# Optimization experiments

Hardware: AMD Instinct MI355X
Metric: run time of the kernel (lower is better)

## Reference

```python
import jax, jax.numpy as jnp
import numpy as np

L = 4
B_LIST = [30, 17, 9, 5, 3]      # bandwidth schedule (geometric 30 -> 3)
F_LIST = [1, 2, 5, 12, 28, 64]  # channel schedule (geometric 1 -> 64)
BATCH = 32
C64 = jnp.complex64

# near-identity grids (beta = pi/16, 6 alphas; SO3 grid additionally 6 gammas)
_A6 = np.linspace(0.0, 2 * np.pi, 6, endpoint=False)
S2_BETA = np.full(6, np.pi / 16)
S2_ALPHA = _A6
_aa, _gg = np.meshgrid(_A6, _A6, indexing='ij')
SO3_ALPHA = _aa.ravel()
SO3_BETA = np.full(36, np.pi / 16)
SO3_GAMMA = _gg.ravel()


def betas_of(b):
    return np.pi * (2 * np.arange(2 * b) + 1) / (4 * b)


def quad_weights(b):
    j = np.arange(2 * b)
    k = np.arange(b)
    s = (np.sin(np.pi * np.outer(2 * j + 1, 2 * k + 1) / (4 * b)) / (2 * k + 1)).sum(1)
    return (2.0 / b) * np.sin(np.pi * (2 * j + 1) / (4 * b)) * s


def wigner_d_all(lmax, betas):
    """Wigner small-d d^l_{m',m}(beta) via exp(-i beta Jy); list_l of [nbeta,2l+1,2l+1]."""
    out = [np.ones((len(betas), 1, 1))]
    for l in range(1, lmax):
        m = np.arange(-l, l)
        jp = np.sqrt(l * (l + 1) - m * (m + 1))  # <m+1|J+|m>
        Jy = np.zeros((2 * l + 1, 2 * l + 1), np.complex128)
        i = np.arange(2 * l)
        Jy[i + 1, i] = -0.5j * jp
        Jy[i, i + 1] = 0.5j * jp
        lam, U = np.linalg.eigh(Jy)
        ph = np.exp(-1j * np.outer(betas, lam))
        out.append(np.einsum('ak,bk,ck->bac', U, ph, U.conj()).real)
    return out


def fft_idx(l, n):
    # indices of frequencies m = -l..l in fft ordering of length n
    return np.concatenate([np.arange(n - l, n), np.arange(l + 1)])


def s2_fft(x, b_out):
    # x: [B,f,2b,2b] real (beta,alpha) -> list_l of [B,f,2l+1] complex
    b_in = x.shape[-1] // 2
    wig = wigner_d_all(b_out, betas_of(b_in))
    w = quad_weights(b_in)
    xf = jnp.fft.fft(x, axis=-1)
    out = []
    for l in range(b_out):
        dl = jnp.asarray((wig[l][:, :, l] * w[:, None]).astype(np.complex64))  # [2b,2l+1]
        out.append(jnp.einsum('bfjm,jm->bfm', xf[..., fft_idx(l, 2 * b_in)], dl))
    return out


def so3_fft(x, b_out):
    # x: [B,f,2b,2b,2b] real (beta,alpha,gamma) -> list_l of [B,f,2l+1,2l+1]
    b_in = x.shape[-1] // 2
    wig = wigner_d_all(b_out, betas_of(b_in))
    w = quad_weights(b_in)
    xf = jnp.fft.fft2(x, axes=(-2, -1))
    out = []
    for l in range(b_out):
        idx = fft_idx(l, 2 * b_in)
        dl = jnp.asarray((wig[l] * w[:, None, None]).astype(np.complex64))
        out.append(jnp.einsum('bfjmn,jmn->bfmn', xf[:, :, :, idx[:, None], idx[None, :]], dl))
    return out


def so3_ifft(coeffs, b):
    # coeffs: list_l [B,f,2l+1,2l+1] -> real signal [B,f,2b,2b,2b]
    wig = wigner_d_all(b, betas_of(b))
    nb = 2 * b
    Bz, f = coeffs[0].shape[:2]
    X = jnp.zeros((Bz, f, nb, nb, nb), C64)
    for l in range(b):
        idx = fft_idx(l, nb)
        dl = jnp.asarray(((2 * l + 1) * wig[l]).astype(np.complex64))
        X = X.at[:, :, :, idx[:, None], idx[None, :]].add(
            jnp.einsum('bfmn,jmn->bfjmn', coeffs[l], dl))
    return (jnp.fft.ifft2(X, axes=(-2, -1)) * (nb * nb)).real


def s2_kernel_ft(k, b):
    # k: [f_in,f_out,P] -> list_l of [2l+1,f_in,f_out] complex
    wig = wigner_d_all(b, S2_BETA)
    kc = k.astype(C64)
    out = []
    for l in range(b):
        m = np.arange(-l, l + 1)
        F = (wig[l][:, :, l] * np.exp(1j * np.outer(S2_ALPHA, m))).astype(np.complex64)
        out.append(jnp.einsum('iop,pm->mio', kc, jnp.asarray(F)))
    return out


def so3_kernel_ft(k, b):
    # k: [f_in,f_out,P] -> list_l of [2l+1,2l+1,f_in,f_out] complex
    wig = wigner_d_all(b, SO3_BETA)
    kc = k.astype(C64)
    out = []
    for l in range(b):
        m = np.arange(-l, l + 1)
        F = (wig[l]
             * np.exp(1j * np.outer(SO3_ALPHA, m))[:, :, None]
             * np.exp(1j * np.outer(SO3_GAMMA, m))[:, None, :]).astype(np.complex64)
        out.append(jnp.einsum('iop,pmn->mnio', kc, jnp.asarray(F)))
    return out


def s2_conv(x, kern, b_out):
    xh = s2_fft(x, b_out)
    kh = s2_kernel_ft(kern, b_out)
    yh = [jnp.einsum('bim,nio->bomn', xh[l], kh[l].conj()) for l in range(b_out)]
    return so3_ifft(yh, b_out)


def so3_conv(x, kern, b_out):
    xh = so3_fft(x, b_out)
    kh = so3_kernel_ft(kern, b_out)
    yh = [jnp.einsum('bimk,nkio->bomn', xh[l], kh[l].conj()) for l in range(b_out)]
    return so3_ifft(yh, b_out)


def so3_integrate(x):
    b = x.shape[-1] // 2
    w = jnp.asarray(quad_weights(b).astype(np.float32))
    return jnp.einsum('bfjac,j->bf', x, w) / float((2 * b) ** 2)


def batchnorm(x, g, be):
    mu = x.mean(0)
    var = ((x - mu) ** 2).mean(0)
    return (x - mu) * jax.lax.rsqrt(var + 1e-5) * g + be


def setup_inputs() -> dict:
    key = jax.random.key(0)
    ks = jax.random.split(key, 10)
    rn = lambda k, s, sc=1.0: jax.random.normal(k, s, jnp.float32) * sc
    return {
        'x': rn(ks[0], (BATCH, 1, 60, 60)),
        'k_s2': rn(ks[1], (1, 2, 6), 0.5),
        'k1': rn(ks[2], (2, 5, 36), 0.1),
        'k2': rn(ks[3], (5, 12, 36), 0.1),
        'k3': rn(ks[4], (12, 28, 36), 0.1),
        'k4': rn(ks[5], (28, 64, 36), 0.1),
        'g1': jnp.ones(64), 'be1': jnp.zeros(64),
        'w1': rn(ks[6], (64, 64), 0.125), 'b1': jnp.zeros(64),
        'g2': jnp.ones(64), 'be2': jnp.zeros(64),
        'w2': rn(ks[7], (64, 32), 0.125), 'b2': jnp.zeros(32),
        'g3': jnp.ones(32), 'be3': jnp.zeros(32),
        'w3': rn(ks[8], (32, 10), 0.18), 'b3': jnp.zeros(10),
    }


def reference(x, k_s2, k1, k2, k3, k4, g1, be1, w1, b1, g2, be2, w2, b2, g3, be3, w3, b3):
    h = jax.nn.relu(s2_conv(x, k_s2, B_LIST[0]))            # [B,2,60,60,60]
    for k, bo in zip((k1, k2, k3, k4), B_LIST[1:]):
        h = jax.nn.relu(so3_conv(h, k, bo))                 # bandwidth shrinks 17,9,5,3
    h = so3_integrate(h)                                    # [B,64]
    h = jax.nn.relu(batchnorm(h, g1, be1) @ w1 + b1)
    h = jax.nn.relu(batchnorm(h, g2, be2) @ w2 + b2)
    return batchnorm(h, g3, be3) @ w3 + b3                  # [B,10]
```

## Files before the change

kernel.cpp:

```cpp
#include <hip/hip_runtime.h>
#include <cmath>
#include <cstring>
#include <vector>


#define DPI 3.14159265358979323846

static constexpr int OQh(int l) { return l*(4*l*l - 1)/3; }
static_assert(OQh(30) == 35990, "oq30");
static_assert(OQh(17) == 6545,  "oq17");
static_assert(OQh(9)  == 969,   "oq9");
static_assert(OQh(5)  == 165,   "oq5");
static_assert(OQh(3)  == 35,    "oq3");

static constexpr int T1SUM = 18445;
static constexpr int T2SUM = 3417;

static constexpr size_t al256(size_t x){ return (x + 255) & ~(size_t)255; }
static constexpr size_t WS_XF1  = 0;
static constexpr size_t WS_XH1  = WS_XF1  + al256(32ull*60*30*8);
static constexpr size_t WS_KH1  = WS_XH1  + al256(32ull*900*8);
static constexpr size_t WS_XT2  = WS_KH1  + al256(1800ull*8);
static constexpr size_t WS_XH2  = WS_XT2  + al256(561ull*3840*8);
static constexpr size_t WS_KH2  = WS_XH2  + al256(64ull*6545*8);
static constexpr size_t WS_YH2T = WS_KH2  + al256(6545ull*10*8);
static constexpr size_t WS_XT3  = WS_YH2T + al256(6545ull*160*8);
static constexpr size_t WS_XH3  = WS_XT3  + al256(153ull*5440*8);
static constexpr size_t WS_KH3  = WS_XH3  + al256(160ull*969*8);
static constexpr size_t WS_YH3T = WS_KH3  + al256(969ull*60*8);
static constexpr size_t WS_XT4  = WS_YH3T + al256(969ull*384*8);
static constexpr size_t WS_XH4  = WS_XT4  + al256(384ull*18*45*8);
static constexpr size_t WS_KH4  = WS_XH4  + al256(384ull*165*8);
static constexpr size_t WS_YH4T = WS_KH4  + al256(165ull*336*8);
static constexpr size_t WS_XT5  = WS_YH4T + al256(165ull*896*8);
static constexpr size_t WS_XH5  = WS_XT5  + al256(896ull*10*15*8);
static constexpr size_t WS_KH5  = WS_XH5  + al256(896ull*35*8);
static constexpr size_t WS_YH5T = WS_KH5  + al256(35ull*1792*8);
static constexpr size_t WS_S5P  = WS_YH5T + al256(35ull*2048*8);
static constexpr size_t WS_RTM  = WS_S5P  + al256(2048ull*6*4);
static constexpr size_t WS_RU   = WS_RTM  + al256(60ull*30*1920*8);
static constexpr size_t WS_TOTAL= WS_RU   + al256(60ull*17*1920*8);

struct ConstOffs {
  size_t A1, dAT2, dAT3, A4, A5;
  size_t dT1, dT2;
  size_t S3, S4, S5;
  size_t WInt;
  size_t nF;
  size_t Fs2, Fso3;
  size_t Tw60, Tw34, Tw18, Tw10, Tw6;
  size_t Wn1, Wn2o, Wn4, Wn5;
  size_t Wg1, Wg2, Wg4;
  size_t WC1, WC2;
  size_t nC;
};
static ConstOffs CO;
static float*  g_devF = nullptr;
static float2* g_devC = nullptr;
static int*    g_devI = nullptr;
static constexpr int IO_TOFF1 = 0;
static constexpr int IO_TOFF2 = 1770;
static constexpr int IO_QOFF2 = 2331;
static constexpr int IO_QLST2 = 2893;
static constexpr int IO_QOFF3 = 9438;
static constexpr int IO_QLST3 = 9592;
static constexpr int IO_TOTAL = 10561;

static void tqli(double* d, double* e, int n, double* z) {
  e[n-1] = 0.0;
  for (int l = 0; l < n; l++) {
    int iter = 0;
    int m;
    do {
      for (m = l; m < n-1; m++) {
        double dd = fabs(d[m]) + fabs(d[m+1]);
        if (fabs(e[m]) <= 1e-300 + 1e-14*dd) break;
      }
      if (m != l) {
        if (iter++ == 80) break;
        double g = (d[l+1]-d[l])/(2.0*e[l]);
        double r = hypot(g, 1.0);
        g = d[m]-d[l]+e[l]/(g + (g >= 0.0 ? fabs(r) : -fabs(r)));
        double s = 1.0, c = 1.0, p = 0.0;
        int i;
        r = 1.0;
        for (i = m-1; i >= l; i--) {
          double f = s*e[i], b = c*e[i];
          r = hypot(f, g);
          e[i+1] = r;
          if (r == 0.0) { d[i+1] -= p; e[m] = 0.0; break; }
          s = f/r; c = g/r;
          g = d[i+1]-p;
          r = (d[i]-g)*s + 2.0*c*b;
          p = s*r;
          d[i+1] = g+p;
          g = c*r-b;
          for (int k = 0; k < n; k++) {
            f = z[(size_t)k*n+i+1];
            z[(size_t)k*n+i+1] = s*z[(size_t)k*n+i] + c*f;
            z[(size_t)k*n+i]   = c*z[(size_t)k*n+i] - s*f;
          }
        }
        if (r == 0.0 && i >= l) continue;
        d[l] -= p; e[l] = g; e[m] = 0.0;
      }
    } while (m != l);
  }
}

struct Builder {
  std::vector<std::vector<double>> V, Lam;
  bool useExpm[30];

  Builder() {
    V.resize(30); Lam.resize(30);
    for (int l = 0; l < 30; l++) {
      int n = 2*l+1;
      std::vector<double> d(n, 0.0), e(n, 0.0), z((size_t)n*n, 0.0);
      for (int i = 0; i < n; i++) z[(size_t)i*n+i] = 1.0;
      for (int i = 0; i+1 < n; i++) {
        double m = (double)i - l;
        e[i] = -0.5*sqrt((double)l*(l+1) - m*(m+1.0));
      }
      if (n > 1) tqli(d.data(), e.data(), n, z.data());
      V[l] = std::move(z); Lam[l] = std::move(d);
    }
    std::vector<double> t((size_t)59*59);
    for (int l = 0; l < 30; l++) {
      useExpm[l] = false;
      if (l == 0) continue;
      int n = 2*l+1;
      eigD(l, 0.77, t.data());
      double corner = pow(cos(0.385), 2.0*l);
      double err = fabs(t[0] - corner) + fabs(t[(size_t)(n-1)*n + (n-1)] - corner);
      double s = 0.0;
      for (int c = 0; c < n; c++) s += t[c]*t[c];
// ... 16 lines not shown
        const double* f = (r & 1) ? sk : ck;
        double s = 0.0;
        for (int k = 0; k < n; k++) s += va[k]*vc[k]*f[k];
        out[(size_t)a*n + c] = (r >= 2) ? -s : s;
      }
    }
  }

  void expmD(int l, double beta, double* out) {
    int n = 2*l+1;
    int s = 0; double bl = fabs(beta)*(double)l + 1e-12;
    while (bl > 0.25) { bl *= 0.5; s++; }
    double sc = ldexp(beta, -s);
    std::vector<double> sup(n > 1 ? n-1 : 0);
    for (int i = 0; i+1 < n; i++) {
      double m = (double)i - l;
      sup[i] = 0.5*sqrt((double)l*(l+1) - m*(m+1.0))*sc;
    }
    std::vector<double> term((size_t)n*n, 0.0), acc((size_t)n*n, 0.0), t2((size_t)n*n);
    for (int i = 0; i < n; i++) { term[(size_t)i*n+i] = 1.0; acc[(size_t)i*n+i] = 1.0; }
    for (int k = 1; k <= 16; k++) {
      for (int r = 0; r < n; r++)
        for (int c = 0; c < n; c++) {
          double v = 0.0;
          if (c > 0)   v += term[(size_t)r*n + c-1]*sup[c-1];
          if (c+1 < n) v -= term[(size_t)r*n + c+1]*sup[c];
          t2[(size_t)r*n+c] = v/(double)k;
        }
      term.swap(t2);
      for (size_t i2 = 0; i2 < (size_t)n*n; i2++) acc[i2] += term[i2];
    }
    for (int t = 0; t < s; t++) {
      for (int r = 0; r < n; r++)
        for (int c = 0; c < n; c++) {
          double v = 0.0;
          for (int k = 0; k < n; k++) v += acc[(size_t)r*n+k]*acc[(size_t)k*n+c];
          t2[(size_t)r*n+c] = v;
        }
      acc.swap(t2);
    }
    std::memcpy(out, acc.data(), sizeof(double)*(size_t)n*n);
  }

  void buildD(int l, double beta, double* out) {
    if (useExpm[l]) expmD(l, beta, out); else eigD(l, beta, out);
  }
};

static std::vector<double> quadw_h(int b) {
  std::vector<double> w(2*b);
  for (int j = 0; j < 2*b; j++) {
    double s = 0;
    for (int k = 0; k < b; k++)
      s += sin(DPI*(2*j+1)*(2*k+1)/(4.0*b))/(double)(2*k+1);
    w[j] = (2.0/b)*sin(DPI*(2*j+1)/(4.0*b))*s;
  }
  return w;
}

static void build_all() {
  size_t o = 0;
  CO.A1   = o; o += 60ull*900;
  CO.dAT2 = o; o += (size_t)OQh(17)*60;
  CO.dAT3 = o; o += (size_t)OQh(9)*34;
  CO.A4   = o; o += 18ull*OQh(5);
  CO.A5   = o; o += 10ull*OQh(3);
  CO.dT1  = o; o += (size_t)T1SUM*60;
  CO.dT2  = o; o += (size_t)T2SUM*34;
  CO.S3   = o; o += 18ull*OQh(9);
  CO.S4   = o; o += 10ull*OQh(5);
  CO.S5   = o; o +=  6ull*OQh(3);
  CO.WInt = o; o += 8;
  CO.nF = o;
  size_t c = 0;
  CO.Fs2  = c; c += 6ull*900;
  CO.Fso3 = c; c += 36ull*OQh(17);
  CO.Tw60 = c; c += 60; CO.Tw34 = c; c += 34;
  CO.Tw18 = c; c += 18; CO.Tw10 = c; c += 10; CO.Tw6 = c; c += 6;
  CO.Wn1  = c; c += 30*60; CO.Wn2o = c; c += 17*34;
  CO.Wn4  = c; c += 5*10;  CO.Wn5  = c; c += 3*6;
  CO.Wg1  = c; c += 60*17; CO.Wg2  = c; c += 34*9; CO.Wg4 = c; c += 10*3;
  CO.WC1  = c; c += 33*60;
  CO.WC2  = c; c += 17*34;
  CO.nC = c;

  std::vector<float> HF(CO.nF, 0.f);
  std::vector<float> HC(2*CO.nC, 0.f);
  std::vector<int> HI(IO_TOTAL, 0);

  { int acc = 0;
    for (int pm = 0; pm < 59; pm++) for (int n = 0; n < 30; n++) {
      int m = pm - 29, am = m < 0 ? -m : m;
      int lm = am > n ? am : n;
      HI[IO_TOFF1 + pm*30 + n] = acc; acc += 30 - lm;
    } }
  { int acc = 0;
    for (int pm = 0; pm < 33; pm++) for (int n = 0; n < 17; n++) {
      int m = pm - 16, am = m < 0 ? -m : m;
      int lm = am > n ? am : n;
      HI[IO_TOFF2 + pm*17 + n] = acc; acc += 17 - lm;
    } }
  { int pos = 0;
    for (int mh = -16; mh <= 16; mh++)
      for (int kh = 0; kh < 17; kh++) {
        HI[IO_QOFF2 + (mh+16)*17 + kh] = pos;
        int am = mh < 0 ? -mh : mh;
        int lmin = am > kh ? am : kh;
        for (int l = lmin; l < 17; l++) {
          int q = OQh(l) + (mh+l)*(2*l+1) + (kh+l);
          HI[IO_QLST2 + pos++] = q*2;
        }
        if (kh > 0)
          for (int l = lmin; l < 17; l++) {
            int q = OQh(l) + (-mh+l)*(2*l+1) + (-kh+l);
            HI[IO_QLST2 + pos++] = q*2 + 1;
          }
      }
    HI[IO_QOFF2 + 561] = pos;
  }
  { int pos = 0;
    for (int mh = -8; mh <= 8; mh++)
      for (int kh = 0; kh < 9; kh++) {
        HI[IO_QOFF3 + (mh+8)*9 + kh] = pos;
        int am = mh < 0 ? -mh : mh;
        int lmin = am > kh ? am : kh;
        for (int l = lmin; l < 9; l++) {
          int q = OQh(l) + (mh+l)*(2*l+1) + (kh+l);
          HI[IO_QLST3 + pos++] = q*2;
        }
        if (kh > 0)
          for (int l = lmin; l < 9; l++) {
            int q = OQh(l) + (-mh+l)*(2*l+1) + (-kh+l);
            HI[IO_QLST3 + pos++] = q*2 + 1;
          }
      }
    HI[IO_QOFF3 + 153] = pos;
  }

  Builder B;
  auto betas = [](int b){ std::vector<double> v(2*b);
    for (int j = 0; j < 2*b; j++) v[j] = DPI*(2*j+1)/(4.0*b); return v; };
  auto w30 = quadw_h(30), w17 = quadw_h(17), w9 = quadw_h(9), w5 = quadw_h(5), w3 = quadw_h(3);
  std::vector<double> tmp((size_t)59*59);

  { auto bs = betas(30);
    for (int l = 0; l < 30; l++) { int W = 2*l+1;
      for (int j = 0; j < 60; j++) {
        B.buildD(l, bs[j], tmp.data());
        for (int mm = -l; mm <= l; mm++)
          for (int nn = 0; nn <= l; nn++) {
            int am = mm < 0 ? -mm : mm;
            int lmin = am > nn ? am : nn;
            int term = HI[IO_TOFF1 + (mm+29)*30 + nn] + (l - lmin);
            HF[CO.dT1 + (size_t)term*60 + j] =
              (float)((2*l+1)*tmp[(size_t)(mm+l)*W + (nn+l)]);
          }
        if (l < 17) {
          for (int rem = 0; rem < W*W; rem++)
            HF[CO.dAT2 + (size_t)(OQh(l)+rem)*60 + j] = (float)(tmp[rem]*w30[j]);
        }
        float* dA1 = HF.data() + CO.A1 + 60ull*l*l + (size_t)j*W;
        for (int mi = 0; mi < W; mi++) dA1[mi] = (float)(tmp[(size_t)mi*W + l]*w30[j]);
      } } }
  { auto bs = betas(17);
    for (int l = 0; l < 17; l++) { int W = 2*l+1;
      for (int j = 0; j < 34; j++) {
// ... 15 lines not shown
      for (int j = 0; j < 18; j++) {
        B.buildD(l, bs[j], tmp.data());
        float* dst = HF.data() + CO.S3 + 18ull*OQh(l) + (size_t)j*W*W;
        for (int i2 = 0; i2 < W*W; i2++) dst[i2] = (float)((2*l+1)*tmp[i2]);
        if (l < 5) {
          float* dA = HF.data() + CO.A4 + 18ull*OQh(l) + (size_t)j*W*W;
          for (int i2 = 0; i2 < W*W; i2++) dA[i2] = (float)(tmp[i2]*w9[j]);
        } } } }
  { auto bs = betas(5);
    for (int l = 0; l < 5; l++) { int W = 2*l+1;
      for (int j = 0; j < 10; j++) {
        B.buildD(l, bs[j], tmp.data());
        float* dst = HF.data() + CO.S4 + 10ull*OQh(l) + (size_t)j*W*W;
        for (int i2 = 0; i2 < W*W; i2++) dst[i2] = (float)((2*l+1)*tmp[i2]);
        if (l < 3) {
          float* dA = HF.data() + CO.A5 + 10ull*OQh(l) + (size_t)j*W*W;
          for (int i2 = 0; i2 < W*W; i2++) dA[i2] = (float)(tmp[i2]*w5[j]);
        } } } }
  { auto bs = betas(3);
    for (int l = 0; l < 3; l++) { int W = 2*l+1;
      for (int j = 0; j < 6; j++) {
        B.buildD(l, bs[j], tmp.data());
        float* dst = HF.data() + CO.S5 + 6ull*OQh(l) + (size_t)j*W*W;
        for (int i2 = 0; i2 < W*W; i2++) dst[i2] = (float)((2*l+1)*tmp[i2]);
      } } }
  { double beta = DPI/16.0;
    for (int l = 0; l < 30; l++) { int n = 2*l+1;
      B.buildD(l, beta, tmp.data());
      for (int p = 0; p < 6; p++) {
        double al = 2.0*DPI*p/6.0;
        for (int mi = 0; mi < n; mi++) {
          double ph = al*(double)(mi - l);
          double dr = tmp[(size_t)mi*n + l];
          size_t off = CO.Fs2 + 6ull*l*l + (size_t)p*n + mi;
          HC[2*off]   = (float)(dr*cos(ph));
          HC[2*off+1] = (float)(dr*sin(ph));
        } }
      if (l < 17) {
        for (int p = 0; p < 36; p++) {
          double al = 2.0*DPI*(p/6)/6.0, ga = 2.0*DPI*(p%6)/6.0;
          for (int mi = 0; mi < n; mi++)
            for (int ni = 0; ni < n; ni++) {
              double ph = al*(double)(mi - l) + ga*(double)(ni - l);
              double dr = tmp[(size_t)mi*n + ni];
              size_t off = CO.Fso3 + 36ull*OQh(l) + (size_t)p*n*n + (size_t)mi*n + ni;
              HC[2*off]   = (float)(dr*cos(ph));
              HC[2*off+1] = (float)(dr*sin(ph));
            } } } } }
  auto fillTw = [&](size_t ofs, int N){
    for (int t = 0; t < N; t++) {
      HC[2*(ofs+t)]   = (float)cos(2.0*DPI*t/N);
      HC[2*(ofs+t)+1] = (float)sin(2.0*DPI*t/N);
    } };
  fillTw(CO.Tw60, 60); fillTw(CO.Tw34, 34);
  fillTw(CO.Tw18, 18); fillTw(CO.Tw10, 10); fillTw(CO.Tw6, 6);
  auto fillWn = [&](size_t ofs, int BQ, int N){
    for (int n = 0; n < BQ; n++)
      for (int cc2 = 0; cc2 < N; cc2++) {
        double f = (n == 0) ? 1.0 : 2.0;
        HC[2*(ofs + (size_t)n*N + cc2)]   = (float)(f*cos(2.0*DPI*n*cc2/N));
        HC[2*(ofs + (size_t)n*N + cc2)+1] = (float)(f*sin(2.0*DPI*n*cc2/N));
      } };
  auto fillWg = [&](size_t ofs, int N, int KT){
    for (int cc2 = 0; cc2 < N; cc2++)
      for (int k = 0; k < KT; k++) {
        HC[2*(ofs + (size_t)cc2*KT + k)]   = (float)cos(2.0*DPI*k*cc2/N);
        HC[2*(ofs + (size_t)cc2*KT + k)+1] = (float)(-sin(2.0*DPI*k*cc2/N));
      } };
  fillWn(CO.Wn1, 30, 60); fillWn(CO.Wn2o, 17, 34);
  fillWn(CO.Wn4, 5, 10);  fillWn(CO.Wn5, 3, 6);
  fillWg(CO.Wg1, 60, 17); fillWg(CO.Wg2, 34, 9); fillWg(CO.Wg4, 10, 3);
  for (int p = 0; p < 33; p++)
    for (int a = 0; a < 60; a++) {
      double th = 2.0*DPI*(p-16)*a/60.0;
      HC[2*(CO.WC1 + (size_t)p*60 + a)]   = (float)cos(th);
      HC[2*(CO.WC1 + (size_t)p*60 + a)+1] = (float)sin(th);
    }
  for (int p = 0; p < 17; p++)
    for (int a = 0; a < 34; a++) {
      double th = 2.0*DPI*(p-8)*a/34.0;
      HC[2*(CO.WC2 + (size_t)p*34 + a)]   = (float)cos(th);
      HC[2*(CO.WC2 + (size_t)p*34 + a)+1] = (float)sin(th);
    }
  for (int j = 0; j < 6; j++) HF[CO.WInt + j] = (float)(w3[j]/36.0);

  size_t fb  = CO.nF * sizeof(float);
  size_t fbA = al256(fb);
  size_t cb  = CO.nC * sizeof(float2);
  size_t cbA = al256(cb);
  size_t ib  = HI.size() * sizeof(int);
  void* base = nullptr;
  if (hipMalloc(&base, fbA + cbA + ib) != hipSuccess || !base) return;
  if (hipMemcpy(base, HF.data(), fb, hipMemcpyHostToDevice) != hipSuccess) return;
  if (hipMemcpy((char*)base + fbA, HC.data(), cb, hipMemcpyHostToDevice) != hipSuccess) return;
  if (hipMemcpy((char*)base + fbA + cbA, HI.data(), ib, hipMemcpyHostToDevice) != hipSuccess) return;
  (void)hipDeviceSynchronize();
  g_devF = (float*)base;
  g_devC = (float2*)((char*)base + fbA);
  g_devI = (int*)((char*)base + fbA + cbA);
}
namespace { struct InitOnce { InitOnce(){ build_all(); } } g_once; }

__device__ __forceinline__ int OQ(int l) { return l*(4*l*l - 1)/3; }
__device__ __forceinline__ int lFromQ(int q, int L) {
  int l = 0;
  while (l+1 < L && OQ(l+1) <= q) l++;
  return l;
}
__device__ __forceinline__ int lsq(int q) {
  int l = (int)sqrtf((float)q);
  while ((l+1)*(l+1) <= q) l++;
  while (l*l > q) l--;
  return l;
}
__device__ __forceinline__ void rotf(float2& r, float2 s) {
  float t = r.x*s.x - r.y*s.y;
  r.y = r.x*s.y + r.y*s.x;
  r.x = t;
}

__device__ __forceinline__ void kh_so3_one(int id, int L, int fi, int fo,
    const float* __restrict__ kk, const float2* __restrict__ F, float2* __restrict__ kh)
{
  int ff = fi*fo;
  int q = id / ff, r = id - q*ff;
  int i = r / fo, o = r - i*fo;
  int l = lFromQ(q, L); int W = 2*l+1; int W21 = W*W;
  int rem = q - OQ(l);
  const float2* Fb = F + 36ull*OQ(l) + rem;
  const float* kb = kk + (size_t)(i*fo + o)*36;
  float ax = 0.f, ay = 0.f;
  for (int p = 0; p < 36; p++) {
    float kv = kb[p];
    float2 f = Fb[(size_t)p*W21];
    ax += kv*f.x; ay += kv*f.y;
  }
  kh[(size_t)q*ff + r] = make_float2(ax, ay);
}

__global__ __launch_bounds__(256) void k_kh_all(
    const float* __restrict__ ks2, const float* __restrict__ k1,
    const float* __restrict__ k2,  const float* __restrict__ k3,
    const float* __restrict__ k4,
    const float2* __restrict__ Fs2, const float2* __restrict__ Fso3,
    float2* __restrict__ kh1, float2* __restrict__ kh2, float2* __restrict__ kh3,
    float2* __restrict__ kh4, float2* __restrict__ kh5)
{
  int id = blockIdx.x*256 + threadIdx.x;
  if (id < 1800) {
    int q = id >> 1, o = id & 1;
    int l = lsq(q); int W = 2*l+1; int mi = q - l*l;
    const float2* Fb = Fs2 + 6ull*l*l;
    float ax = 0.f, ay = 0.f;
    for (int p = 0; p < 6; p++) {
      float kv = ks2[o*6 + p];
      float2 f = Fb[p*W + mi];
      ax += kv*f.x; ay += kv*f.y;
    }
    kh1[(size_t)q*2 + o] = make_float2(ax, ay);
    return;
  }
  id -= 1800;
  if (id < OQh(17)*10) { kh_so3_one(id, 17, 2, 5, k1, Fso3, kh2); return; }
  id -= OQh(17)*10;
  if (id < OQh(9)*60) { kh_so3_one(id, 9, 5, 12, k2, Fso3, kh3); return; }
  id -= OQh(9)*60;
  if (id < OQh(5)*336) { kh_so3_one(id, 5, 12, 28, k3, Fso3, kh4); return; }
  id -= OQh(5)*336;
  if (id < OQh(3)*1792) { kh_so3_one(id, 3, 28, 64, k4, Fso3, kh5); return; }
}

__global__ __launch_bounds__(64) void k_s1_fftA(
    const float* __restrict__ x, const float2* __restrict__ tw, float2* __restrict__ XF1)
{
  __shared__ float row[60];
  int b = blockIdx.x / 60, j = blockIdx.x - b*60;
  int t = threadIdx.x;
  if (t < 60) row[t] = x[((size_t)b*60 + j)*60 + t];
  __syncthreads();
  if (t < 30) {
    float ax = 0.f, ay = 0.f;
    int ti = 0;
    for (int a = 0; a < 60; a++) {
      float2 w = tw[ti];
      ax += row[a]*w.x; ay -= row[a]*w.y;
      ti += t; if (ti >= 60) ti -= 60;
    }
    XF1[((size_t)b*60 + j)*30 + t] = make_float2(ax, ay);
  }
}

__global__ __launch_bounds__(256) void k_s1_coef(
    const float2* __restrict__ XF1, const float* __restrict__ dA1, float2* __restrict__ xh1)
{
  int id = blockIdx.x*blockDim.x + threadIdx.x;
  if (id >= 32*900) return;
  int b = id / 900, q = id - b*900;
  int l = lsq(q); int W = 2*l+1; int mi = q - l*l; int m = mi - l;
  const float* dp = dA1 + 60ull*l*l + mi;
  const float2* xb = XF1 + (size_t)b*60*30;
  int ma = m >= 0 ? m : -m;
  float sg = m >= 0 ? 1.f : -1.f;
  float ax = 0.f, ay = 0.f;
  for (int j = 0; j < 60; j++) {
    float2 xf = xb[j*30 + ma];
    float d = dp[(size_t)j*W];
    ax += d*xf.x; ay += sg*d*xf.y;
  }
  xh1[id] = make_float2(ax, ay);
}

__global__ __launch_bounds__(256) void k_yh_t(
    const float2* __restrict__ xh, const float2* __restrict__ kh,
    float2* __restrict__ yht, int L, int fi, int fo, int Qtot)
{
  int id = blockIdx.x*256 + threadIdx.x;
  int BOF = 32*fo;
  if (id >= Qtot*BOF) return;
  int q = id / BOF, bo = id - q*BOF;
  int b = bo / fo, o = bo - b*fo;
  int l = lFromQ(q, L); int W = 2*l+1;
  int rem = q - OQ(l); int mi = rem / W, ni = rem - mi*W;
  int ff = fi*fo;
  const float2* xb = xh + ((size_t)b*fi)*Qtot + OQ(l) + mi*W;
  const float2* kb = kh + ((size_t)(OQ(l) + ni*W))*ff + o;
  float ax = 0.f, ay = 0.f;
  for (int i = 0; i < fi; i++) {
    const float2* xrow = xb + (size_t)i*Qtot;
    const float2* krow = kb + (size_t)i*fo;
    for (int k = 0; k < W; k++) {
      float2 xv = xrow[k];
      float2 kv = krow[(size_t)k*ff];
      ax += xv.x*kv.x + xv.y*kv.y;
      ay += xv.y*kv.x - xv.x*kv.y;
    }
  }
  yht[id] = make_float2(ax, ay);
}

template<int BQ, int NJ, int BO, int CHSL, int STAGE1>
__global__ __launch_bounds__(64) void k_scatA(
    const float2* __restrict__ src,
    const float2* __restrict__ khp,
    const float* __restrict__ dT, const int* __restrict__ toff,
    const float2* __restrict__ twN, float2* __restrict__ Tm, int slBase)
{
  constexpr int W2 = 2*BQ - 1;
  constexpr int N  = 2*BQ;
  constexpr int NAH = BQ;
  __shared__ float2 P[W2*64];
  __shared__ float2 twl[N];
  __shared__ float2 kc[STAGE1 ? 2*BQ : 2];
  const int lane = threadIdx.x;
  constexpr int TILES = CHSL/64;
  int n = blockIdx.x / TILES, ts = blockIdx.x - n*TILES;
  int slL = ts*64 + lane;
  int slG = slBase + slL;
  int bo = slG / NJ;
  int j  = slG - bo*NJ;

  if (lane < N) twl[lane] = twN[lane];
  if constexpr (STAGE1) {
    int cnt = 2*(BQ - n);
    if (lane < cnt) {
      int l = n + (lane >> 1), o = lane & 1;
      kc[2*l + o] = khp[(size_t)(l*l + n + l)*2 + o];
    }
  }
  __syncthreads();

  for (int pm = 0; pm < W2; pm++) {
    int m = pm - (BQ-1);
    int am = m < 0 ? -m : m;
    int lmin = am > n ? am : n;
    int K = BQ - lmin;
    int tof = toff[pm*BQ + n];
    const float* dp = dT + (size_t)tof*NJ + j;
    float ax = 0.f, ay = 0.f;
    if constexpr (STAGE1) {
      int b = bo >> 1, o = bo & 1;
      const float2* xb = src + (size_t)b*900;
      for (int li = 0; li < K; li++) {
        int l = lmin + li;
        float d = dp[(size_t)li*NJ];
        float2 xv = xb[l*l + m + l];
        float2 kv = kc[2*l + o];
        float yx = xv.x*kv.x + xv.y*kv.y;
        float yy = xv.y*kv.x - xv.x*kv.y;
        ax = fmaf(d, yx, ax); ay = fmaf(d, yy, ay);
      }
    } else {
      for (int li = 0; li < K; li++) {
        int l = lmin + li;
        int e = OQ(l) + (m+l)*(2*l+1) + (n+l);
        float d = dp[(size_t)li*NJ];
        float2 y = src[(size_t)e*BO + bo];
        ax = fmaf(d, y.x, ax); ay = fmaf(d, y.y, ay);
      }
    }
    P[pm*64 + lane] = make_float2(ax, ay);
  }
  __syncthreads();

  float2 E[NAH], Od[NAH];
  #pragma unroll
  for (int a = 0; a < NAH; a++) { E[a] = make_float2(0.f,0.f); Od[a] = make_float2(0.f,0.f); }
  for (int t2 = 0; t2 < BQ; t2++) {
    int pm = 2*t2;
    float2 p = P[pm*64 + lane];
    int s = pm - (BQ-1); if (s < 0) s += N;
    int idx = 0;
    #pragma unroll
    for (int a = 0; a < NAH; a++) {
      float2 w = twl[idx];
      E[a].x = fmaf(p.x, w.x, fmaf(-p.y, w.y, E[a].x));
      E[a].y = fmaf(p.x, w.y, fmaf( p.y, w.x, E[a].y));
      idx += s; if (idx >= N) idx -= N;
    }
  }
  for (int t2 = 0; t2 < BQ-1; t2++) {
    int pm = 2*t2 + 1;
    float2 p = P[pm*64 + lane];
    int s = pm - (BQ-1); if (s < 0) s += N;
    int idx = 0;
    #pragma unroll
    for (int a = 0; a < NAH; a++) {
      float2 w = twl[idx];
      Od[a].x = fmaf(p.x, w.x, fmaf(-p.y, w.y, Od[a].x));
      Od[a].y = fmaf(p.x, w.y, fmaf( p.y, w.x, Od[a].y));
      idx += s; if (idx >= N) idx -= N;
    }
  }
  constexpr bool QS = ((BQ-1) & 1) != 0;
  #pragma unroll
  for (int a = 0; a < NAH; a++) {
    float2 tp = make_float2(E[a].x + Od[a].x, E[a].y + Od[a].y);
    float2 tq = QS ? make_float2(Od[a].x - E[a].x, Od[a].y - E[a].y)
                   : make_float2(E[a].x - Od[a].x, E[a].y - Od[a].y);
    Tm[((size_t)a*BQ + n)*CHSL + slL] = tp;
    Tm[((size_t)(a+NAH)*BQ + n)*CHSL + slL] = tq;
  }
}

template<int BQ, int KT, int CHSL>
__global__ __launch_bounds__(64) void k_dftB(
    const float2* __restrict__ Tm, const float2* __restrict__ Wn,
    const float2* __restrict__ Wg, float2* __restrict__ U)
{
  constexpr int N = 2*BQ;
  constexpr int NH = BQ;
  __shared__ float2 WnL[BQ*NH];
  __shared__ float2 WgL[NH*KT];
  constexpr int TILES = CHSL/64;
  int a = blockIdx.x / TILES, ts = blockIdx.x - a*TILES;
  int lane = threadIdx.x;
  for (int i = lane; i < BQ*NH; i += 64) { int nn = i/NH, c = i - nn*NH; WnL[i] = Wn[(size_t)nn*N + c]; }
  for (int i = lane; i < NH*KT; i += 64) WgL[i] = Wg[i];
  __syncthreads();
  int sl = ts*64 + lane;
  float SE[NH], SO[NH];
  #pragma unroll
  for (int c = 0; c < NH; c++) { SE[c] = 0.f; SO[c] = 0.f; }
  const float2* Tb = Tm + (size_t)a*BQ*CHSL + sl;
  for (int t2 = 0; 2*t2 < BQ; t2++) {
    int nn = 2*t2;
    float2 tv = Tb[(size_t)nn*CHSL];
    #pragma unroll
    for (int c = 0; c < NH; c++) {
      float2 w = WnL[nn*NH + c];
      SE[c] = fmaf(tv.x, w.x, fmaf(-tv.y, w.y, SE[c]));
    }
  }
  for (int t2 = 0; 2*t2+1 < BQ; t2++) {
    int nn = 2*t2 + 1;
    float2 tv = Tb[(size_t)nn*CHSL];
    #pragma unroll
    for (int c = 0; c < NH; c++) {
      float2 w = WnL[nn*NH + c];
      SO[c] = fmaf(tv.x, w.x, fmaf(-tv.y, w.y, SO[c]));
    }
  }
  #pragma unroll
  for (int c = 0; c < NH; c++) {
    float s0 = fmaxf(SE[c] + SO[c], 0.f);
    float s1 = fmaxf(SE[c] - SO[c], 0.f);
    SE[c] = s0 + s1;
    SO[c] = s0 - s1;
  }
  float2* Ub = U + (size_t)a*KT*CHSL + sl;
  for (int k = 0; k < KT; k += 2) {
    float ux = 0.f, uy = 0.f;
    #pragma unroll
    for (int c = 0; c < NH; c++) {
      float2 w = WgL[c*KT + k];
      ux = fmaf(SE[c], w.x, ux); uy = fmaf(SE[c], w.y, uy);
    }
    Ub[(size_t)k*CHSL] = make_float2(ux, uy);
  }
  for (int k = 1; k < KT; k += 2) {
    float ux = 0.f, uy = 0.f;
    #pragma unroll
    for (int c = 0; c < NH; c++) {
      float2 w = WgL[c*KT + k];
      ux = fmaf(SO[c], w.x, ux); uy = fmaf(SO[c], w.y, uy);
    }
    Ub[(size_t)k*CHSL] = make_float2(ux, uy);
  }
}

template<int MT, int KT, int NH, int CHSL>
__global__ __launch_bounds__(64) void k_dftC(
    const float2* __restrict__ U, const float2* __restrict__ WC,
    float2* __restrict__ xt, int slOff, int SLfull)
{
  constexpr int NA = 2*NH;
  __shared__ float2 WcL[NH*MT];
  constexpr int TILES = CHSL/64;
  int k = blockIdx.x / TILES, ts = blockIdx.x - k*TILES;
  int lane = threadIdx.x;
  for (int i = lane; i < NH*MT; i += 64) { int aa = i/MT, p = i - aa*MT; WcL[i] = WC[(size_t)p*NA + aa]; }
  __syncthreads();
  int sl = ts*64 + lane;
  float2 acc[MT];
  #pragma unroll
  for (int p = 0; p < MT; p++) acc[p] = make_float2(0.f, 0.f);
  const float2* Ubk = U + (size_t)k*CHSL + sl;
  for (int aa = 0; aa < NH; aa++) {
    float2 u  = Ubk[(size_t)aa*KT*CHSL];
    float2 u2 = Ubk[(size_t)(aa+NH)*KT*CHSL];
    float2 vp = make_float2(u.x + u2.x, u.y + u2.y);
    float2 vm = make_float2(u.x - u2.x, u.y - u2.y);
    const float2* wr = &WcL[aa*MT];
    #pragma unroll
    for (int p = 0; p < MT; p++) {
      float2 w = wr[p];
      float2 v = (p & 1) ? vm : vp;
      acc[p].x = fmaf(v.x, w.x, fmaf( v.y, w.y, acc[p].x));
      acc[p].y = fmaf(v.y, w.x, fmaf(-v.x, w.y, acc[p].y));
    }
  }
  #pragma unroll
  for (int p = 0; p < MT; p++)
    xt[((size_t)(p*KT + k))*SLfull + slOff + sl] = acc[p];
}

template<int NBI, int NJ, int PAD, int QTOT>
__global__ __launch_bounds__(256) void k_coefg(
    const float2* __restrict__ xt, const float* __restrict__ dAT,
    const int* __restrict__ qoff, const int* __restrict__ qlist,
    float2* __restrict__ xh, int SLfull)
{
  __shared__ float re[NBI*PAD], im[NBI*PAD];
  int pr = blockIdx.x;
  const float2* row = xt + (size_t)pr*SLfull;
  for (int idx = threadIdx.x; idx < NBI*NJ; idx += 256) {
    int bi = idx / NJ, j = idx - bi*NJ;
    float2 v = row[idx];
    re[bi*PAD + j] = v.x; im[bi*PAD + j] = v.y;
  }
  __syncthreads();
  int o0 = qoff[pr], nq = qoff[pr+1] - o0;
  int w = threadIdx.x >> 6, lane = threadIdx.x & 63;
  for (int i = w; i < nq; i += 4) {
    int e = qlist[o0 + i];
    int q = e >> 1;
    float sg = (e & 1) ? -1.f : 1.f;
    const float* dp = dAT + (size_t)q*NJ;
    for (int bi = lane; bi < NBI; bi += 64) {
      float ax = 0.f, ay = 0.f;
      const float* rr = &re[bi*PAD];
      const float* ii = &im[bi*PAD];
      #pragma unroll 4
      for (int j = 0; j < NJ; j++) {
        float d = dp[j];
        ax = fmaf(d, rr[j], ax);
        ay = fmaf(d, ii[j], ay);
      }
      xh[(size_t)bi*QTOT + q] = make_float2(ax, sg*ay);
    }
  }
}

__global__ __launch_bounds__(256) void k_coef(
    const float2* __restrict__ xt, const float* __restrict__ dA,
    float2* __restrict__ xh, int L, int nj, int KT, int MT, int Qtot, int nbi)
{
  int id = blockIdx.x*blockDim.x + threadIdx.x;
  if (id >= nbi*Qtot) return;
  int bi = id / Qtot, q = id - bi*Qtot;
  int l = lFromQ(q, L); int W = 2*l+1; int W21 = W*W;
  int rem = q - OQ(l); int mi = rem / W, ki = rem - mi*W;
  int m = mi - l, ks = ki - l;
  const float* dAp = dA + (size_t)nj*OQ(l) + rem;
  int MTKT = MT*KT;
  int pidx; float sgn;
  if (ks >= 0) { pidx = (m + (KT-1))*KT + ks;  sgn =  1.f; }
  else         { pidx = (-m + (KT-1))*KT - ks; sgn = -1.f; }
  const float2* xb = xt + (size_t)bi*nj*MTKT + pidx;
  float ax = 0.f, ay = 0.f;
  for (int j = 0; j < nj; j++) {
    float2 xv = xb[(size_t)j*MTKT];
    float d = dAp[(size_t)j*W21];
    ax += d*xv.x; ay += sgn*d*xv.y;
  }
  xh[id] = make_float2(ax, ay);
}

template<int BQ, int N, int KT, int MT, int TPB, int BO>
__global__ __launch_bounds__(TPB) void k_synth3(
    const float2* __restrict__ yh, const float* __restrict__ dS,
    const float2* __restrict__ twN, float2* __restrict__ xt)
{
  constexpr int W2  = 2*BQ - 1;
  constexpr int NH  = N/2;
  constexpr int CP  = (BQ+3) & ~3;
  constexpr int KTP = (KT+1) & ~1;
  constexpr int R3  = (N%4 == 0) ? 4 : 2;
  constexpr int RP  = (NH%2 == 0) ? 2 : 1;
  constexpr int SZA0 = (W2*CP*8 > 2*N*NH*4) ? W2*CP*8 : 2*N*NH*4;
  constexpr int SZA  = (SZA0 + 15) & ~15;
  constexpr int SZB0 = (N*CP*8 > 2*NH*KTP*8) ? N*CP*8 : 2*NH*KTP*8;
  constexpr int SZB  = (SZB0 + 15) & ~15;
  __shared__ __align__(16) char smem[SZA + SZB + N*8];
  float2* P   = (float2*)smem;
  float*  SS  = (float*)smem;
  float*  SD  = SS + N*NH;
// ... 360 lines not shown
    for (int f = 0; f < 64; f++) s += Bs[b*64+f]*w2[f*32+fo];
    C[idx] = fmaxf(s, 0.f);
  }
  __syncthreads();
  if (tid < 32) {
    float m = 0.f; for (int b = 0; b < 32; b++) m += C[b*32+tid]; m *= (1.f/32);
    float v = 0.f; for (int b = 0; b < 32; b++) { float d = C[b*32+tid]-m; v += d*d; } v *= (1.f/32);
    mu[tid] = m; iv[tid] = rsqrtf(v + 1e-5f)*g3[tid];
  }
  __syncthreads();
  for (int idx = tid; idx < 1024; idx += 256) {
    int f = idx & 31;
    C[idx] = (C[idx]-mu[f])*iv[f] + be3[f];
  }
  __syncthreads();
  for (int idx = tid; idx < 320; idx += 256) {
    int b = idx/10, cc = idx - b*10;
    float s = b3[cc];
    for (int f = 0; f < 32; f++) s += C[b*32+f]*w3[f*10+cc];
    out[idx] = s;
  }
}

static inline int cdiv_h(int a, int b) { return (a + b - 1)/b; }

extern "C" void kernel_launch(void* const* d_in, const int* in_sizes, int n_in,
                              void* d_out, int out_size, void* d_ws, size_t ws_size,
                              hipStream_t stream) {
  (void)in_sizes; (void)n_in; (void)out_size;
  if (!g_devF || !g_devC || !g_devI || ws_size < WS_TOTAL) return;

  const float* x    = (const float*)d_in[0];
  const float* ks2  = (const float*)d_in[1];
  const float* k1   = (const float*)d_in[2];
  const float* k2   = (const float*)d_in[3];
  const float* k3   = (const float*)d_in[4];
  const float* k4   = (const float*)d_in[5];
  const float* g1   = (const float*)d_in[6],  *be1 = (const float*)d_in[7];
  const float* w1   = (const float*)d_in[8],  *b1  = (const float*)d_in[9];
  const float* g2   = (const float*)d_in[10], *be2 = (const float*)d_in[11];
  const float* w2   = (const float*)d_in[12], *b2  = (const float*)d_in[13];
  const float* g3   = (const float*)d_in[14], *be3 = (const float*)d_in[15];
  const float* w3   = (const float*)d_in[16], *b3  = (const float*)d_in[17];
  float* out = (float*)d_out;
  char* ws = (char*)d_ws;

  float2* XF1  = (float2*)(ws + WS_XF1);
  float2* xh1  = (float2*)(ws + WS_XH1);
  float2* kh1  = (float2*)(ws + WS_KH1);
  float2* xt2  = (float2*)(ws + WS_XT2);
  float2* xh2  = (float2*)(ws + WS_XH2);
  float2* kh2  = (float2*)(ws + WS_KH2);
  float2* yh2t = (float2*)(ws + WS_YH2T);
  float2* xt3  = (float2*)(ws + WS_XT3);
  float2* xh3  = (float2*)(ws + WS_XH3);
  float2* kh3  = (float2*)(ws + WS_KH3);
  float2* yh3t = (float2*)(ws + WS_YH3T);
  float2* xt4  = (float2*)(ws + WS_XT4);
  float2* xh4  = (float2*)(ws + WS_XH4);
  float2* kh4  = (float2*)(ws + WS_KH4);
  float2* yh4t = (float2*)(ws + WS_YH4T);
  float2* xt5  = (float2*)(ws + WS_XT5);
  float2* xh5  = (float2*)(ws + WS_XH5);
  float2* kh5  = (float2*)(ws + WS_KH5);
  float2* yh5t = (float2*)(ws + WS_YH5T);
  float*  s5p  = (float*) (ws + WS_S5P);
  float2* RTm  = (float2*)(ws + WS_RTM);
  float2* RU   = (float2*)(ws + WS_RU);

  const float* dA1p  = g_devF + CO.A1;
  const float* dAT2p = g_devF + CO.dAT2;
  const float* dAT3p = g_devF + CO.dAT3;
  const float* dA4p  = g_devF + CO.A4;
  const float* dA5p  = g_devF + CO.A5;
  const float* dT1p  = g_devF + CO.dT1;
  const float* dT2p  = g_devF + CO.dT2;
  const float* dS3p  = g_devF + CO.S3;
  const float* dS4p  = g_devF + CO.S4;
  const float* dS5p  = g_devF + CO.S5;
  const float* wIntp = g_devF + CO.WInt;
  const float2* Fs2p  = g_devC + CO.Fs2;
  const float2* Fso3p = g_devC + CO.Fso3;
  const float2* tw60p = g_devC + CO.Tw60;
  const float2* tw34p = g_devC + CO.Tw34;
  const float2* tw18p = g_devC + CO.Tw18;
  const float2* tw10p = g_devC + CO.Tw10;
  const float2* tw6p  = g_devC + CO.Tw6;
  const float2* Wn1p  = g_devC + CO.Wn1;
  const float2* Wn2p  = g_devC + CO.Wn2o;
  const float2* Wn4p  = g_devC + CO.Wn4;
  const float2* Wn5p  = g_devC + CO.Wn5;
  const float2* Wg1p  = g_devC + CO.Wg1;
  const float2* Wg2p  = g_devC + CO.Wg2;
  const float2* Wg4p  = g_devC + CO.Wg4;
  const float2* WC1p  = g_devC + CO.WC1;
  const float2* WC2p  = g_devC + CO.WC2;
  const int* toff1p  = g_devI + IO_TOFF1;
  const int* toff2p  = g_devI + IO_TOFF2;
  const int* qoff2p  = g_devI + IO_QOFF2;
  const int* qlist2p = g_devI + IO_QLST2;
  const int* qoff3p  = g_devI + IO_QOFF3;
  const int* qlist3p = g_devI + IO_QLST3;

  constexpr int Q17 = OQh(17), Q9 = OQh(9), Q5 = OQh(5), Q3 = OQh(3);

  k_kh_all<<<952, 256, 0, stream>>>(ks2, k1, k2, k3, k4, Fs2p, Fso3p,
                                    kh1, kh2, kh3, kh4, kh5);

  k_s1_fftA<<<32*60, 64, 0, stream>>>(x, tw60p, XF1);
  k_s1_coef<<<cdiv_h(32*900,256), 256, 0, stream>>>(XF1, dA1p, xh1);

  for (int c = 0; c < 2; c++) {
    int base = c*1920;
    k_scatA<30,60,64,1920,1><<<30*30, 64, 0, stream>>>(xh1, kh1, dT1p, toff1p, tw60p, RTm, base);
    k_dftB<30,17,1920><<<60*30, 64, 0, stream>>>(RTm, Wn1p, Wg1p, RU);
    k_dftC<33,17,30,1920><<<17*30, 64, 0, stream>>>(RU, WC1p, xt2, base, 3840);
  }
  k_coefg<64,60,61,Q17><<<561, 256, 0, stream>>>(xt2, dAT2p, qoff2p, qlist2p, xh2, 3840);
  k_yh_t<<<cdiv_h(Q17*160,256), 256, 0, stream>>>(xh2, kh2, yh2t, 17, 2, 5, Q17);

  k_scatA<17,34,160,5440,0><<<17*85, 64, 0, stream>>>(yh2t, nullptr, dT2p, toff2p, tw34p, RTm, 0);
  k_dftB<17,9,5440><<<34*85, 64, 0, stream>>>(RTm, Wn2p, Wg2p, RU);
  k_dftC<17,9,17,5440><<<9*85, 64, 0, stream>>>(RU, WC2p, xt3, 0, 5440);

  k_coefg<160,34,35,Q9><<<153, 256, 0, stream>>>(xt3, dAT3p, qoff3p, qlist3p, xh3, 5440);
  k_yh_t<<<cdiv_h(Q9*384,256), 256, 0, stream>>>(xh3, kh3, yh3t, 9, 5, 12, Q9);

  k_synth3<9,18,5,9,64,384><<<384*18, 64, 0, stream>>>(yh3t, dS3p, tw18p, xt4);
  k_coef<<<cdiv_h(384*Q5,256), 256, 0, stream>>>(xt4, dA4p, xh4, 5, 18, 5, 9, Q5, 384);
  k_yh_t<<<cdiv_h(Q5*896,256), 256, 0, stream>>>(xh4, kh4, yh4t, 5, 12, 28, Q5);

  k_synth2<5,10,3,5,0,1,64,896><<<896*10, 64, 0, stream>>>(yh4t, dS4p, tw10p, Wn4p, Wg4p, xt5, nullptr, nullptr);
  k_coef<<<cdiv_h(896*Q3,256), 256, 0, stream>>>(xt5, dA5p, xh5, 3, 10, 3, 5, Q3, 896);
  k_yh_t<<<cdiv_h(Q3*2048,256), 256, 0, stream>>>(xh5, kh5, yh5t, 3, 28, 64, Q3);

  k_synth2<3,6,3,5,1,1,64,2048><<<2048*6, 64, 0, stream>>>(yh5t, dS5p, tw6p, Wn5p, nullptr, nullptr, s5p, wIntp);

  k_mlp<<<1, 256, 0, stream>>>(s5p, g1, be1, w1, b1, g2, be2, w2, b2, g3, be3, w3, b3, out);
}
```

Baseline: 928.6 us.

## Split scatter and DFT kernels across four wavefronts with shared twiddle tables

Moves the scatter, dftB and dftC stages of the SO(3) synthesis from one-wave 64-thread blocks to 256-thread blocks. Each wave handles a slice of the output columns or pm rows, which cuts per-thread register arrays (E/Od, acc) from BQ or MT entries to about a quarter. The scatter kernel now reads a precomputed even/odd twiddle matrix from shared memory instead of doing modular index arithmetic. dftC stages its U inputs in shared memory. This is meant to reduce register pressure and raise occupancy, at the cost of more shared memory per block and some redundant loads.

```diff
diff --git a/kernel.cpp b/kernel.cpp
--- a/kernel.cpp
+++ b/kernel.cpp
@@ -52,6 +52,7 @@
   size_t Wn1, Wn2o, Wn4, Wn5;
   size_t Wg1, Wg2, Wg4;
   size_t WC1, WC2;
+  size_t WEO1, WEO2;
   size_t nC;
 };
 static ConstOffs CO;
@@ -234,6 +235,8 @@
   CO.Wg1  = c; c += 60*17; CO.Wg2  = c; c += 34*9; CO.Wg4 = c; c += 10*3;
   CO.WC1  = c; c += 33*60;
   CO.WC2  = c; c += 17*34;
+  CO.WEO1 = c; c += 59*30;
+  CO.WEO2 = c; c += 33*17;
   CO.nC = c;
 
   std::vector<float> HF(CO.nF, 0.f);
@@ -415,6 +418,20 @@
       HC[2*(CO.WC2 + (size_t)p*34 + a)]   = (float)cos(th);
       HC[2*(CO.WC2 + (size_t)p*34 + a)+1] = (float)sin(th);
     }
+  for (int pm = 0; pm < 59; pm++)
+    for (int a = 0; a < 30; a++) {
+      int s = ((pm - 29) % 60 + 60) % 60;
+      double th = 2.0*DPI*a*s/60.0;
+      HC[2*(CO.WEO1 + (size_t)pm*30 + a)]   = (float)cos(th);
+      HC[2*(CO.WEO1 + (size_t)pm*30 + a)+1] = (float)sin(th);
+    }
+  for (int pm = 0; pm < 33; pm++)
+    for (int a = 0; a < 17; a++) {
+      int s = ((pm - 16) % 34 + 34) % 34;
+      double th = 2.0*DPI*a*s/34.0;
+      HC[2*(CO.WEO2 + (size_t)pm*17 + a)]   = (float)cos(th);
+      HC[2*(CO.WEO2 + (size_t)pm*17 + a)+1] = (float)sin(th);
+    }
   for (int j = 0; j < 6; j++) HF[CO.WInt + j] = (float)(w3[j]/36.0);
 
   size_t fb  = CO.nF * sizeof(float);
@@ -572,37 +589,37 @@
 }
 
 template<int BQ, int NJ, int BO, int CHSL, int STAGE1>
-__global__ __launch_bounds__(64) void k_scatA(
+__global__ __launch_bounds__(256) void k_scatB(
     const float2* __restrict__ src,
     const float2* __restrict__ khp,
     const float* __restrict__ dT, const int* __restrict__ toff,
-    const float2* __restrict__ twN, float2* __restrict__ Tm, int slBase)
+    const float2* __restrict__ WEO, float2* __restrict__ Tm, int slBase)
 {
   constexpr int W2 = 2*BQ - 1;
-  constexpr int N  = 2*BQ;
-  constexpr int NAH = BQ;
+  constexpr int TILES = CHSL/64;
+  constexpr int PG = (BQ + 3)/4;
   __shared__ float2 P[W2*64];
-  __shared__ float2 twl[N];
-  __shared__ float2 kc[STAGE1 ? 2*BQ : 2];
-  const int lane = threadIdx.x;
-  constexpr int TILES = CHSL/64;
+  __shared__ float2 Wl[W2*BQ];
+  __shared__ float2 kcl[STAGE1 ? 2*BQ : 2];
+  const int tid = threadIdx.x;
+  const int g = tid >> 6, lane = tid & 63;
   int n = blockIdx.x / TILES, ts = blockIdx.x - n*TILES;
   int slL = ts*64 + lane;
   int slG = slBase + slL;
   int bo = slG / NJ;
   int j  = slG - bo*NJ;
 
-  if (lane < N) twl[lane] = twN[lane];
+  for (int i = tid; i < W2*BQ; i += 256) Wl[i] = WEO[i];
   if constexpr (STAGE1) {
     int cnt = 2*(BQ - n);
-    if (lane < cnt) {
-      int l = n + (lane >> 1), o = lane & 1;
-      kc[2*l + o] = khp[(size_t)(l*l + n + l)*2 + o];
-    }
-  }
-  __syncthreads();
-
-  for (int pm = 0; pm < W2; pm++) {
+    if (tid < cnt) {
+      int l = n + (tid >> 1), o = tid & 1;
+      kcl[2*l + o] = khp[(size_t)(l*l + n + l)*2 + o];
+    }
+  }
+  __syncthreads();
+
+  for (int pm = g; pm < W2; pm += 4) {
     int m = pm - (BQ-1);
     int am = m < 0 ? -m : m;
     int lmin = am > n ? am : n;
@@ -617,7 +634,7 @@
         int l = lmin + li;
         float d = dp[(size_t)li*NJ];
         float2 xv = xb[l*l + m + l];
-        float2 kv = kc[2*l + o];
+        float2 kv = kcl[2*l + o];
         float yx = xv.x*kv.x + xv.y*kv.y;
         float yy = xv.y*kv.x - xv.x*kv.y;
         ax = fmaf(d, yx, ax); ay = fmaf(d, yy, ay);
@@ -635,61 +652,60 @@
   }
   __syncthreads();
 
-  float2 E[NAH], Od[NAH];
+  int a0 = g*PG;
+  int cnt = BQ - a0; if (cnt > PG) cnt = PG; if (cnt < 0) cnt = 0;
+  float2 E[PG], Od[PG];
   #pragma unroll
-  for (int a = 0; a < NAH; a++) { E[a] = make_float2(0.f,0.f); Od[a] = make_float2(0.f,0.f); }
+  for (int i = 0; i < PG; i++) { E[i] = make_float2(0.f,0.f); Od[i] = make_float2(0.f,0.f); }
   for (int t2 = 0; t2 < BQ; t2++) {
-    int pm = 2*t2;
-    float2 p = P[pm*64 + lane];
-    int s = pm - (BQ-1); if (s < 0) s += N;
-    int idx = 0;
+    float2 p = P[(2*t2)*64 + lane];
+    const float2* wr = &Wl[(2*t2)*BQ + a0];
     #pragma unroll
-    for (int a = 0; a < NAH; a++) {
-      float2 w = twl[idx];
-      E[a].x = fmaf(p.x, w.x, fmaf(-p.y, w.y, E[a].x));
-      E[a].y = fmaf(p.x, w.y, fmaf( p.y, w.x, E[a].y));
-      idx += s; if (idx >= N) idx -= N;
+    for (int i = 0; i < PG; i++) {
+      float2 w = wr[i];
+      E[i].x = fmaf(p.x, w.x, fmaf(-p.y, w.y, E[i].x));
+      E[i].y = fmaf(p.x, w.y, fmaf( p.y, w.x, E[i].y));
     }
   }
   for (int t2 = 0; t2 < BQ-1; t2++) {
-    int pm = 2*t2 + 1;
-    float2 p = P[pm*64 + lane];
-    int s = pm - (BQ-1); if (s < 0) s += N;
-    int idx = 0;
+    float2 p = P[(2*t2+1)*64 + lane];
+    const float2* wr = &Wl[(2*t2+1)*BQ + a0];
     #pragma unroll
-    for (int a = 0; a < NAH; a++) {
-      float2 w = twl[idx];
-      Od[a].x = fmaf(p.x, w.x, fmaf(-p.y, w.y, Od[a].x));
-      Od[a].y = fmaf(p.x, w.y, fmaf( p.y, w.x, Od[a].y));
-      idx += s; if (idx >= N) idx -= N;
+    for (int i = 0; i < PG; i++) {
+      float2 w = wr[i];
+      Od[i].x = fmaf(p.x, w.x, fmaf(-p.y, w.y, Od[i].x));
+      Od[i].y = fmaf(p.x, w.y, fmaf( p.y, w.x, Od[i].y));
     }
   }
   constexpr bool QS = ((BQ-1) & 1) != 0;
-  #pragma unroll
-  for (int a = 0; a < NAH; a++) {
-    float2 tp = make_float2(E[a].x + Od[a].x, E[a].y + Od[a].y);
-    float2 tq = QS ? make_float2(Od[a].x - E[a].x, Od[a].y - E[a].y)
-                   : make_float2(E[a].x - Od[a].x, E[a].y - Od[a].y);
+  for (int i = 0; i < cnt; i++) {
+    int a = a0 + i;
+    float2 tp = make_float2(E[i].x + Od[i].x, E[i].y + Od[i].y);
+    float2 tq = QS ? make_float2(Od[i].x - E[i].x, Od[i].y - E[i].y)
+                   : make_float2(E[i].x - Od[i].x, E[i].y - Od[i].y);
     Tm[((size_t)a*BQ + n)*CHSL + slL] = tp;
-    Tm[((size_t)(a+NAH)*BQ + n)*CHSL + slL] = tq;
+    Tm[((size_t)(a+BQ)*BQ + n)*CHSL + slL] = tq;
   }
 }
 
 template<int BQ, int KT, int CHSL>
-__global__ __launch_bounds__(64) void k_dftB(
+__global__ __launch_bounds__(256) void k_dftB2(
     const float2* __restrict__ Tm, const float2* __restrict__ Wn,
     const float2* __restrict__ Wg, float2* __restrict__ U)
 {
   constexpr int N = 2*BQ;
   constexpr int NH = BQ;
+  constexpr int TILES = CHSL/64;
   __shared__ float2 WnL[BQ*NH];
   __shared__ float2 WgL[NH*KT];
-  constexpr int TILES = CHSL/64;
-  int a = blockIdx.x / TILES, ts = blockIdx.x - a*TILES;
-  int lane = threadIdx.x;
-  for (int i = lane; i < BQ*NH; i += 64) { int nn = i/NH, c = i - nn*NH; WnL[i] = Wn[(size_t)nn*N + c]; }
-  for (int i = lane; i < NH*KT; i += 64) WgL[i] = Wg[i];
-  __syncthreads();
+  int a4 = blockIdx.x / TILES, ts = blockIdx.x - a4*TILES;
+  int tid = threadIdx.x;
+  int g = tid >> 6, lane = tid & 63;
+  int a = a4*4 + g;
+  for (int i = tid; i < BQ*NH; i += 256) { int nn = i/NH, c = i - nn*NH; WnL[i] = Wn[(size_t)nn*N + c]; }
+  for (int i = tid; i < NH*KT; i += 256) WgL[i] = Wg[i];
+  __syncthreads();
+  if (a >= N) return;
   int sl = ts*64 + lane;
   float SE[NH], SO[NH];
   #pragma unroll
@@ -742,39 +758,48 @@
 }
 
 template<int MT, int KT, int NH, int CHSL>
-__global__ __launch_bounds__(64) void k_dftC(
+__global__ __launch_bounds__(256) void k_dftC2(
     const float2* __restrict__ U, const float2* __restrict__ WC,
     float2* __restrict__ xt, int slOff, int SLfull)
 {
   constexpr int NA = 2*NH;
+  constexpr int TILES = CHSL/64;
+  constexpr int PGp = (MT + 3)/4;
+  __shared__ float2 Us[NA*64];
   __shared__ float2 WcL[NH*MT];
-  constexpr int TILES = CHSL/64;
   int k = blockIdx.x / TILES, ts = blockIdx.x - k*TILES;
-  int lane = threadIdx.x;
-  for (int i = lane; i < NH*MT; i += 64) { int aa = i/MT, p = i - aa*MT; WcL[i] = WC[(size_t)p*NA + aa]; }
-  __syncthreads();
-  int sl = ts*64 + lane;
-  float2 acc[MT];
+  int tid = threadIdx.x;
+  int g = tid >> 6, lane = tid & 63;
+  for (int i = tid; i < NA*64; i += 256) {
+    int aa = i >> 6, ll = i & 63;
+    Us[i] = U[((size_t)aa*KT + k)*CHSL + ts*64 + ll];
+  }
+  for (int i = tid; i < NH*MT; i += 256) { int aa = i/MT, p = i - aa*MT; WcL[i] = WC[(size_t)p*NA + aa]; }
+  __syncthreads();
+  int p0 = g*PGp;
+  int cnt = MT - p0; if (cnt > PGp) cnt = PGp; if (cnt < 0) cnt = 0;
+  float2 acc[PGp];
   #pragma unroll
-  for (int p = 0; p < MT; p++) acc[p] = make_float2(0.f, 0.f);
-  const float2* Ubk = U + (size_t)k*CHSL + sl;
+  for (int i = 0; i < PGp; i++) acc[i] = make_float2(0.f, 0.f);
   for (int aa = 0; aa < NH; aa++) {
-    float2 u  = Ubk[(size_t)aa*KT*CHSL];
-    float2 u2 = Ubk[(size_t)(aa+NH)*KT*CHSL];
+    float2 u  = Us[aa*64 + lane];
+    float2 u2 = Us[(aa+NH)*64 + lane];
     float2 vp = make_float2(u.x + u2.x, u.y + u2.y);
     float2 vm = make_float2(u.x - u2.x, u.y - u2.y);
-    const float2* wr = &WcL[aa*MT];
+    const float2* wr = &WcL[aa*MT + p0];
     #pragma unroll
-    for (int p = 0; p < MT; p++) {
-      float2 w = wr[p];
-      float2 v = (p & 1) ? vm : vp;
-      acc[p].x = fmaf(v.x, w.x, fmaf( v.y, w.y, acc[p].x));
-      acc[p].y = fmaf(v.y, w.x, fmaf(-v.x, w.y, acc[p].y));
-    }
-  }
-  #pragma unroll
-  for (int p = 0; p < MT; p++)
-    xt[((size_t)(p*KT + k))*SLfull + slOff + sl] = acc[p];
+    for (int i = 0; i < PGp; i++) {
+      float2 w = wr[i];
+      float2 v = ((p0 + i) & 1) ? vm : vp;
+      acc[i].x = fmaf(v.x, w.x, fmaf( v.y, w.y, acc[i].x));
+      acc[i].y = fmaf(v.y, w.x, fmaf(-v.x, w.y, acc[i].y));
+    }
+  }
+  int sl = ts*64 + lane;
+  for (int i = 0; i < cnt; i++) {
+    int p = p0 + i;
+    xt[((size_t)(p*KT + k))*SLfull + slOff + sl] = acc[i];
+  }
 }
 
 template<int NBI, int NJ, int PAD, int QTOT>
@@ -1301,7 +1326,6 @@
   const float2* Fs2p  = g_devC + CO.Fs2;
   const float2* Fso3p = g_devC + CO.Fso3;
   const float2* tw60p = g_devC + CO.Tw60;
-  const float2* tw34p = g_devC + CO.Tw34;
   const float2* tw18p = g_devC + CO.Tw18;
   const float2* tw10p = g_devC + CO.Tw10;
   const float2* tw6p  = g_devC + CO.Tw6;
@@ -1314,6 +1338,8 @@
   const float2* Wg4p  = g_devC + CO.Wg4;
   const float2* WC1p  = g_devC + CO.WC1;
   const float2* WC2p  = g_devC + CO.WC2;
+  const float2* WEO1p = g_devC + CO.WEO1;
+  const float2* WEO2p = g_devC + CO.WEO2;
   const int* toff1p  = g_devI + IO_TOFF1;
   const int* toff2p  = g_devI + IO_TOFF2;
   const int* qoff2p  = g_devI + IO_QOFF2;
@@ -1331,16 +1357,16 @@
 
   for (int c = 0; c < 2; c++) {
     int base = c*1920;
-    k_scatA<30,60,64,1920,1><<<30*30, 64, 0, stream>>>(xh1, kh1, dT1p, toff1p, tw60p, RTm, base);
-    k_dftB<30,17,1920><<<60*30, 64, 0, stream>>>(RTm, Wn1p, Wg1p, RU);
-    k_dftC<33,17,30,1920><<<17*30, 64, 0, stream>>>(RU, WC1p, xt2, base, 3840);
+    k_scatB<30,60,64,1920,1><<<30*30, 256, 0, stream>>>(xh1, kh1, dT1p, toff1p, WEO1p, RTm, base);
+    k_dftB2<30,17,1920><<<15*30, 256, 0, stream>>>(RTm, Wn1p, Wg1p, RU);
+    k_dftC2<33,17,30,1920><<<17*30, 256, 0, stream>>>(RU, WC1p, xt2, base, 3840);
   }
   k_coefg<64,60,61,Q17><<<561, 256, 0, stream>>>(xt2, dAT2p, qoff2p, qlist2p, xh2, 3840);
   k_yh_t<<<cdiv_h(Q17*160,256), 256, 0, stream>>>(xh2, kh2, yh2t, 17, 2, 5, Q17);
 
-  k_scatA<17,34,160,5440,0><<<17*85, 64, 0, stream>>>(yh2t, nullptr, dT2p, toff2p, tw34p, RTm, 0);
-  k_dftB<17,9,5440><<<34*85, 64, 0, stream>>>(RTm, Wn2p, Wg2p, RU);
-  k_dftC<17,9,17,5440><<<9*85, 64, 0, stream>>>(RU, WC2p, xt3, 0, 5440);
+  k_scatB<17,34,160,5440,0><<<17*85, 256, 0, stream>>>(yh2t, nullptr, dT2p, toff2p, WEO2p, RTm, 0);
+  k_dftB2<17,9,5440><<<9*85, 256, 0, stream>>>(RTm, Wn2p, Wg2p, RU);
+  k_dftC2<17,9,17,5440><<<9*85, 256, 0, stream>>>(RU, WC2p, xt3, 0, 5440);
 
   k_coefg<160,34,35,Q9><<<153, 256, 0, stream>>>(xt3, dAT3p, qoff3p, qlist3p, xh3, 5440);
   k_yh_t<<<cdiv_h(Q9*384,256), 256, 0, stream>>>(xh3, kh3, yh3t, 9, 5, 12, Q9);
```

New measurement: 825.6 us. -11.1%, faster.
